# Kernel optimization log

Hardware: AMD Instinct MI355X
Metric: run time of the kernel (lower is better)

The kernel has to match this reference:

```python
import jax, jax.numpy as jnp
import numpy as np

HEADS = 16
DIM_HEAD = 64
EPS = 1e-8
MASK_VALUE = -np.finfo(np.float32).max


def rotate_half(x):
    # x: [..., rot_dim]; split into two halves (j=2 grouping) and rotate
    x1, x2 = jnp.split(x.reshape(*x.shape[:-1], 2, x.shape[-1] // 2), 2, axis=-2)
    x1 = x1.squeeze(-2)
    x2 = x2.squeeze(-2)
    return jnp.concatenate((-x2, x1), axis=-1)


def apply_rotary_pos_emb(t, freqs):
    # t: [b, h, n, d], freqs: [n, rot_dim]
    rot_dim = freqs.shape[-1]
    t_rot, t_pass = t[..., :rot_dim], t[..., rot_dim:]
    t_rot = t_rot * jnp.cos(freqs) + rotate_half(t_rot) * jnp.sin(freqs)
    return jnp.concatenate((t_rot, t_pass), axis=-1)


def setup_inputs() -> dict:
    key = jax.random.key(0)
    ks = jax.random.split(key, 6)
    b, n, dim = 2, 2048, 1024
    inner = HEADS * DIM_HEAD
    rot_dim = 32
    return {
        "x": jax.random.normal(ks[0], (b, n, dim), jnp.float32),
        "freqs": jax.random.normal(ks[1], (n, rot_dim), jnp.float32),
        "gamma": jnp.ones((dim,), jnp.float32),
        "Wq": jax.random.normal(ks[2], (dim, inner), jnp.float32) * (dim ** -0.5),
        "Wkv": jax.random.normal(ks[3], (dim, 2 * inner), jnp.float32) * (dim ** -0.5),
        "Wo": jax.random.normal(ks[4], (inner, dim), jnp.float32) * (inner ** -0.5),
        "bo": jnp.zeros((dim,), jnp.float32),
    }


def reference(x, freqs, gamma, Wq, Wkv, Wo, bo):
    b, n, dim = x.shape
    scale = DIM_HEAD ** -0.5

    # RMSNorm (norm-based formulation, matching the torch code)
    norm = jnp.linalg.norm(x, axis=-1, keepdims=True) * (dim ** -0.5)
    xn = x / jnp.maximum(norm, EPS) * gamma

    q = xn @ Wq                      # [b, n, h*d]
    kv = xn @ Wkv                    # [b, n, 2*h*d]
    k, v = jnp.split(kv, 2, axis=-1)

    def to_heads(t):
        return t.reshape(b, n, HEADS, DIM_HEAD).transpose(0, 2, 1, 3)  # [b,h,n,d]

    q, k, v = map(to_heads, (q, k, v))
    q = q * scale

    q = apply_rotary_pos_emb(q, freqs)
    k = apply_rotary_pos_emb(k, freqs)

    sim = jnp.einsum('bhid,bhjd->bhij', q, k)
    causal_mask = jnp.triu(jnp.ones((n, n), bool), k=1)
    sim = jnp.where(causal_mask, MASK_VALUE, sim)

    attn = jax.nn.softmax(sim, axis=-1)
    out = jnp.einsum('bhij,bhjd->bhid', attn, v)
    out = out.transpose(0, 2, 1, 3).reshape(b, n, HEADS * DIM_HEAD)
    return out @ Wo + bo
```

## Files before the change

### kernel.cpp

```cpp
#include <hip/hip_runtime.h>
#include <hip/hip_bf16.h>
#include <math.h>

typedef short s8 __attribute__((ext_vector_type(8)));
typedef float f4 __attribute__((ext_vector_type(4)));

#define HEADS 16
#define DHEAD 64
#define NSEQ 2048
#define BATCH 2
#define DIM 1024
#define ROT 32
#define QSCALE 0.18033688011112042f

static __device__ __forceinline__ unsigned short f2bf(float f) {
    union { float f; unsigned int u; } v; v.f = f;
    unsigned int u = v.u;
    unsigned int r = (u + 0x7FFFu + ((u >> 16) & 1u)) >> 16;
    return (unsigned short)r;
}

static __device__ __forceinline__ unsigned int cvt_pk_bf16(float lo, float hi) {
    unsigned int r;
    asm volatile("v_cvt_pk_bf16_f32 %0, %1, %2" : "=v"(r) : "v"(lo), "v"(hi));
    return r;
}

static __device__ __forceinline__ void gload_lds16(
        const unsigned short* g, unsigned short* l) {
    __builtin_amdgcn_global_load_lds(
        (const __attribute__((address_space(1))) void*)g,
        (__attribute__((address_space(3))) void*)l,
        16, 0, 0);
}

static __device__ __forceinline__ void tr_tile(
        const float* __restrict__ in, unsigned short* __restrict__ out,
        int K, int N, int n0, int k0, int tid, float* tile ) {
    int tx = tid & 31, ty = tid >> 5;
    #pragma unroll
    for (int j = 0; j < 32; j += 8)
        tile[(ty + j) * 33 + tx] = in[(size_t)(k0 + ty + j) * N + n0 + tx];
    __syncthreads();
    #pragma unroll
    for (int j = 0; j < 32; j += 8)
        out[(size_t)(n0 + ty + j) * K + k0 + tx] = f2bf(tile[tx * 33 + ty + j]);
}

__global__ __launch_bounds__(256) void prep_rms_kernel(
        const float* __restrict__ x, const float* __restrict__ gamma,
        const float* __restrict__ Wq, const float* __restrict__ Wkv,
        const float* __restrict__ Wo, const float* __restrict__ freqs,
        unsigned short* __restrict__ xn, unsigned short* __restrict__ WqT,
        unsigned short* __restrict__ WkvT, unsigned short* __restrict__ WoT,
        float* __restrict__ cs) {
    __shared__ float smem[32 * 33];
    int bid = blockIdx.x, tid = threadIdx.x;
    if (bid < 4096) {
        int row = bid;
        float4 v = ((const float4*)(x + (size_t)row * DIM))[tid];
        float ss = v.x * v.x + v.y * v.y + v.z * v.z + v.w * v.w;
        #pragma unroll
        for (int m = 1; m < 64; m <<= 1) ss += __shfl_xor(ss, m, 64);
        int wave = tid >> 6;
        if ((tid & 63) == 0) smem[wave] = ss;
        __syncthreads();
        float total = smem[0] + smem[1] + smem[2] + smem[3];
        float norm = sqrtf(total * (1.0f / DIM));
        float inv = 1.0f / fmaxf(norm, 1e-8f);
        float4 g = ((const float4*)gamma)[tid];
        ushort4 o;
        o.x = f2bf(v.x * inv * g.x);
        o.y = f2bf(v.y * inv * g.y);
        o.z = f2bf(v.z * inv * g.z);
        o.w = f2bf(v.w * inv * g.w);
        ((ushort4*)(xn + (size_t)row * DIM))[tid] = o;
    } else if (bid < 5120) {
        int idx = bid - 4096;
        tr_tile(Wq, WqT, 1024, 1024, (idx & 31) * 32, (idx >> 5) * 32, tid, smem);
    } else if (bid < 7168) {
        int idx = bid - 5120;
        tr_tile(Wkv, WkvT, 1024, 2048, (idx & 63) * 32, (idx >> 6) * 32, tid, smem);
    } else if (bid < 8192) {
        int idx = bid - 7168;
        tr_tile(Wo, WoT, 1024, 1024, (idx & 31) * 32, (idx >> 5) * 32, tid, smem);
    } else {
        int i = (bid - 8192) * 256 + tid;
        int npos = i >> 6, j = i & 63;
        int q = j >> 4;
        int fi = (q >> 1) * 16 + (j & 15);
        float f = freqs[npos * ROT + fi];
        cs[i] = (q & 1) ? sinf(f) : cosf(f);
    }
}

#define GEMM_COMPUTE(AOFF, BOFF)                                                        \
    {                                                                                   \
        s8 a0 = *(const s8*)(ar + (AOFF));                                              \
        s8 a1 = *(const s8*)(ar + (AOFF) + 512);                                        \
        s8 b0 = *(const s8*)(br + (BOFF));                                              \
        s8 b1 = *(const s8*)(br + (BOFF) + 512);                                        \
        s8 b2 = *(const s8*)(br + (BOFF) + 1024);                                       \
        s8 b3 = *(const s8*)(br + (BOFF) + 1536);                                       \
        acc[0][0] = __builtin_amdgcn_mfma_f32_16x16x32_bf16(a0, b0, acc[0][0], 0, 0, 0);\
        acc[0][1] = __builtin_amdgcn_mfma_f32_16x16x32_bf16(a0, b1, acc[0][1], 0, 0, 0);\
        acc[0][2] = __builtin_amdgcn_mfma_f32_16x16x32_bf16(a0, b2, acc[0][2], 0, 0, 0);\
        acc[0][3] = __builtin_amdgcn_mfma_f32_16x16x32_bf16(a0, b3, acc[0][3], 0, 0, 0);\
        acc[1][0] = __builtin_amdgcn_mfma_f32_16x16x32_bf16(a1, b0, acc[1][0], 0, 0, 0);\
        acc[1][1] = __builtin_amdgcn_mfma_f32_16x16x32_bf16(a1, b1, acc[1][1], 0, 0, 0);\
        acc[1][2] = __builtin_amdgcn_mfma_f32_16x16x32_bf16(a1, b2, acc[1][2], 0, 0, 0);\
        acc[1][3] = __builtin_amdgcn_mfma_f32_16x16x32_bf16(a1, b3, acc[1][3], 0, 0, 0);\
    }

#define GEMM_FENCE()                                             \
    asm volatile("s_waitcnt vmcnt(0)" ::: "memory");             \
    __builtin_amdgcn_s_barrier();                                \
    __builtin_amdgcn_sched_barrier(0);

static __device__ __forceinline__ void gemm_core64_db(
        const unsigned short* __restrict__ A, const unsigned short* __restrict__ BT,
        int bm0, int bn0, unsigned short* As, unsigned short* Bs, f4 acc[2][4]) {
    const int Kd = DIM;
    int tid = threadIdx.x, lane = tid & 63, w = tid >> 6;
    int wr = w >> 1, wc = w & 1;
    int r16 = lane & 15, g8 = 8 * (lane >> 4);
    int srow = lane >> 2, scol = (lane & 3) * 8;
    const unsigned short* Ag0 = A  + (size_t)(bm0 + w * 16 + srow) * Kd + scol;
    const unsigned short* Bg0 = BT + (size_t)(bn0 + (w * 2 + 0) * 16 + srow) * Kd + scol;
    const unsigned short* Bg1 = BT + (size_t)(bn0 + (w * 2 + 1) * 16 + srow) * Kd + scol;
    unsigned short* Al  = As + w * 512;
    unsigned short* Bl0 = Bs + (w * 2 + 0) * 512;
    unsigned short* Bl1 = Bs + (w * 2 + 1) * 512;
    const unsigned short* ar = As + (wr * 32 + r16) * 32 + g8;
    const unsigned short* br = Bs + (wc * 64 + r16) * 32 + g8;
    gload_lds16(Ag0, Al);
    gload_lds16(Bg0, Bl0);
    gload_lds16(Bg1, Bl1);
    GEMM_FENCE();
    for (int t = 0; t < 32; t += 2) {
        {
            int k1 = (t + 1) * 32;
            gload_lds16(Ag0 + k1, Al + 2048);
            gload_lds16(Bg0 + k1, Bl0 + 4096);
            gload_lds16(Bg1 + k1, Bl1 + 4096);
        }
        GEMM_COMPUTE(0, 0);
        GEMM_FENCE();
        if (t + 2 < 32) {
            int k2 = (t + 2) * 32;
            gload_lds16(Ag0 + k2, Al);
            gload_lds16(Bg0 + k2, Bl0);
            gload_lds16(Bg1 + k2, Bl1);
        }
        GEMM_COMPUTE(2048, 4096);
        GEMM_FENCE();
    }
}

__global__ __launch_bounds__(256) void gemm_qkv(
        const unsigned short* __restrict__ xn, const unsigned short* __restrict__ WqT,
        const unsigned short* __restrict__ WkvT, const float* __restrict__ cs,
        unsigned short* __restrict__ q_h, unsigned short* __restrict__ k_h,
        unsigned short* __restrict__ v_t) {
    __shared__ unsigned short As[2 * 64 * 32];
    __shared__ unsigned short Bs[2 * 128 * 32];
    f4 acc[2][4];
    #pragma unroll
    for (int m = 0; m < 2; ++m)
        #pragma unroll
        for (int n = 0; n < 4; ++n) acc[m][n] = 0.f;
    int bx = blockIdx.x;
    bool isq = (bx < 8);
    int bm0 = blockIdx.y * 64;
    int bn0 = (isq ? bx : (bx - 8)) * 128;
    gemm_core64_db(xn, isq ? WqT : WkvT, bm0, bn0, As, Bs, acc);
    int lane = threadIdx.x & 63, w = threadIdx.x >> 6;
    int wr = w >> 1, wc = w & 1, g = lane >> 4, c0 = lane & 15;
    if (isq) {
        int h = 2 * bx + wc;
        #pragma unroll
        for (int m = 0; m < 2; ++m)
            #pragma unroll
            for (int r = 0; r < 4; ++r) {
                int row = bm0 + wr * 32 + m * 16 + 4 * g + r;
                int b = row >> 11, npos = row & 2047;
                const float* csr = cs + npos * 64;
                float a0 = acc[m][0][r] * QSCALE;
                float a1 = acc[m][1][r] * QSCALE;
                float q0 = a0 * csr[c0] - a1 * csr[16 + c0];
                float q1 = a1 * csr[32 + c0] + a0 * csr[48 + c0];
                unsigned short* dst = q_h + ((size_t)(b * HEADS + h) * NSEQ + npos) * DHEAD;
                dst[c0]      = f2bf(q0);
                dst[16 + c0] = f2bf(q1);
                dst[32 + c0] = f2bf(acc[m][2][r] * QSCALE);
                dst[48 + c0] = f2bf(acc[m][3][r] * QSCALE);
            }
    } else if (bx < 16) {
        int h = 2 * (bx - 8) + wc;
        #pragma unroll
        for (int m = 0; m < 2; ++m)
            #pragma unroll
            for (int r = 0; r < 4; ++r) {
                int row = bm0 + wr * 32 + m * 16 + 4 * g + r;
                int b = row >> 11, npos = row & 2047;
                const float* csr = cs + npos * 64;
                float a0 = acc[m][0][r], a1 = acc[m][1][r];
                float k0v = a0 * csr[c0] - a1 * csr[16 + c0];
                float k1v = a1 * csr[32 + c0] + a0 * csr[48 + c0];
                unsigned short* dst = k_h + ((size_t)(b * HEADS + h) * NSEQ + npos) * DHEAD;
                dst[c0]      = f2bf(k0v);
                dst[16 + c0] = f2bf(k1v);
                dst[32 + c0] = f2bf(acc[m][2][r]);
                dst[48 + c0] = f2bf(acc[m][3][r]);
            }
    } else {
        int h = 2 * (bx - 16) + wc;
        #pragma unroll
        for (int m = 0; m < 2; ++m) {
            int row0 = bm0 + wr * 32 + m * 16 + 4 * g;
            int b = row0 >> 11, npos0 = row0 & 2047;
            unsigned short* vb = v_t + (size_t)(b * HEADS + h) * DHEAD * NSEQ;
            #pragma unroll
            for (int n = 0; n < 4; ++n) {
                uint2 pk;
                pk.x = cvt_pk_bf16(acc[m][n][0], acc[m][n][1]);
                pk.y = cvt_pk_bf16(acc[m][n][2], acc[m][n][3]);
                *(uint2*)(vb + (size_t)(n * 16 + c0) * NSEQ + npos0) = pk;
            }
        }
    }
}

#define PSTRIDE 72

static __device__ __forceinline__ void stage_kv64(
        const unsigned short* __restrict__ kb, const unsigned short* __restrict__ vb,
        int j0, unsigned short* Kd, unsigned short* Vd, int w, int lane) {
    int r8 = lane >> 3, c = lane & 7;
    int sc = c ^ r8;
    #pragma unroll
    for (int i = 0; i < 2; ++i) {
        int rb = (w * 2 + i) * 8;
        int r = rb + r8;
        gload_lds16(kb + (size_t)(j0 + r) * DHEAD + sc * 8, Kd + rb * DHEAD);
        gload_lds16(vb + (size_t)r * NSEQ + j0 + sc * 8,    Vd + rb * DHEAD);
    }
}

template<bool MASKT>
static __device__ __forceinline__ void attn_tile_lds(
        int j0, int q0, int g, int c0, int njt,
        const unsigned short* Kc, const unsigned short* Vc,
        s8 qf0, s8 qf1, unsigned short* plw,
        f4 o[4], float& m, float& l) {
    int sw = c0 & 7;
    int off0 = ((g ^ sw) << 3);
    int off1 = (((g + 4) ^ sw) << 3);
    f4 s[4];
    #pragma unroll
    for (int jt = 0; jt < 4; ++jt) {
        f4 acc; acc = 0.f;
        if (!MASKT || jt < njt) {
            const unsigned short* kp = Kc + (jt * 16 + c0) * DHEAD;
            s8 kf0 = *(const s8*)(kp + off0);
            s8 kf1 = *(const s8*)(kp + off1);
            acc = __builtin_amdgcn_mfma_f32_16x16x32_bf16(kf0, qf0, acc, 0, 0, 0);
            acc = __builtin_amdgcn_mfma_f32_16x16x32_bf16(kf1, qf1, acc, 0, 0, 0);
        }
        s[jt] = acc;
    }
    if (MASKT) {
        #pragma unroll
        for (int jt = 0; jt < 4; ++jt)
            #pragma unroll
            for (int r = 0; r < 4; ++r) {
                int j = j0 + jt * 16 + 4 * g + r;
                if (j > q0 + c0) s[jt][r] = -1e30f;
            }
    }
    f4 mv = s[0];
    #pragma unroll
    for (int jt = 1; jt < 4; ++jt)
        #pragma unroll
        for (int r = 0; r < 4; ++r) mv[r] = fmaxf(mv[r], s[jt][r]);
    float mx = fmaxf(fmaxf(mv[0], mv[1]), fmaxf(mv[2], mv[3]));
    mx = fmaxf(mx, __shfl_xor(mx, 16));
    mx = fmaxf(mx, __shfl_xor(mx, 32));
    if (__any(mx > m + 11.5f)) {
        float mnew = fmaxf(m, mx);
        float alpha = exp2f(m - mnew);
        l *= alpha;
        #pragma unroll
        for (int dc = 0; dc < 4; ++dc)
            #pragma unroll
            for (int r = 0; r < 4; ++r) o[dc][r] *= alpha;
        m = mnew;
    }
    float rs = 0.f;
    unsigned int* prow = (unsigned int*)(plw + c0 * PSTRIDE);
    #pragma unroll
    for (int jt = 0; jt < 4; ++jt) {
        f4 p;
        #pragma unroll
        for (int r = 0; r < 4; ++r) { p[r] = exp2f(s[jt][r] - m); rs += p[r]; }
        uint2 pk;
        pk.x = cvt_pk_bf16(p[0], p[1]);
        pk.y = cvt_pk_bf16(p[2], p[3]);
        ((uint2*)prow)[jt * 4 + g] = pk;
    }
    rs += __shfl_xor(rs, 16);
    rs += __shfl_xor(rs, 32);
    l += rs;
    __builtin_amdgcn_sched_barrier(0);
    asm volatile("s_waitcnt lgkmcnt(0)" ::: "memory");
    __builtin_amdgcn_sched_barrier(0);
    const unsigned short* prd = plw + c0 * PSTRIDE + 8 * g;
    s8 pf0 = *(const s8*)(prd);
    s8 pf1 = *(const s8*)(prd + 32);
    bool hi_half = (!MASKT) || (njt > 2);
    #pragma unroll
    for (int dc = 0; dc < 4; ++dc) {
        const unsigned short* vp = Vc + (dc * 16 + c0) * DHEAD;
        s8 vf0 = *(const s8*)(vp + off0);
        o[dc] = __builtin_amdgcn_mfma_f32_16x16x32_bf16(vf0, pf0, o[dc], 0, 0, 0);
        if (hi_half) {
            s8 vf1 = *(const s8*)(vp + off1);
            o[dc] = __builtin_amdgcn_mfma_f32_16x16x32_bf16(vf1, pf1, o[dc], 0, 0, 0);
        }
    }
}

__global__ __launch_bounds__(256) void attn_kernel(
        const unsigned short* __restrict__ q_h, const unsigned short* __restrict__ k_h,
        const unsigned short* __restrict__ v_t, unsigned short* __restrict__ attn_out) {
    __shared__ unsigned short Ks[2][64 * DHEAD];
    __shared__ unsigned short Vs[2][64 * DHEAD];
    __shared__ unsigned short p_lds[4][16][PSTRIDE];
    int tid = threadIdx.x, lane = tid & 63, w = tid >> 6;
    int g = lane >> 4, c0 = lane & 15;
    int bid = blockIdx.x;
    int k = bid >> 3;
    int qt = 31 - (k >> 2);
    int bh = (bid & 7) + ((k & 3) << 3);
    const unsigned short* qb = q_h + (size_t)bh * NSEQ * DHEAD;
    const unsigned short* kb = k_h + (size_t)bh * NSEQ * DHEAD;
    const unsigned short* vb = v_t + (size_t)bh * DHEAD * NSEQ;
    unsigned short* plw = &p_lds[w][0][0];
    int b = bh >> 4, h = bh & 15;
    int q0 = qt * 64 + w * 16;
    s8 qf0 = *(const s8*)(qb + (size_t)(q0 + c0) * DHEAD + 8 * g);
    s8 qf1 = *(const s8*)(qb + (size_t)(q0 + c0) * DHEAD + 32 + 8 * g);
    f4 o[4]; o[0] = 0.f; o[1] = 0.f; o[2] = 0.f; o[3] = 0.f;
    float m = -1e30f, l = 0.f;
    int nt = qt + 1;
    stage_kv64(kb, vb, 0, Ks[0], Vs[0], w, lane);
    __syncthreads();
    for (int t = 0; t < nt; ++t) {
        const unsigned short* Kc = Ks[t & 1];
        const unsigned short* Vc = Vs[t & 1];
        if (t + 1 < nt)
            stage_kv64(kb, vb, (t + 1) * 64, Ks[(t + 1) & 1], Vs[(t + 1) & 1], w, lane);
        if (t == nt - 1)
            attn_tile_lds<true>(t * 64, q0, g, c0, w + 1, Kc, Vc, qf0, qf1, plw, o, m, l);
        else
            attn_tile_lds<false>(t * 64, q0, g, c0, 4, Kc, Vc, qf0, qf1, plw, o, m, l);
        __syncthreads();
    }
    float invl = 1.0f / l;
    unsigned short* dst = attn_out + ((size_t)(b * NSEQ) + q0 + c0) * (HEADS * DHEAD) + h * DHEAD;
    #pragma unroll
    for (int dc = 0; dc < 4; ++dc) {
        uint2 pk;
        pk.x = cvt_pk_bf16(o[dc][0] * invl, o[dc][1] * invl);
        pk.y = cvt_pk_bf16(o[dc][2] * invl, o[dc][3] * invl);
        *(uint2*)(dst + dc * 16 + 4 * g) = pk;
    }
}

__global__ __launch_bounds__(256) void gemm_o(
        const unsigned short* __restrict__ attn, const unsigned short* __restrict__ WoT,
        const float* __restrict__ bo, float* __restrict__ out) {
    __shared__ unsigned short As[2 * 64 * 32];
    __shared__ unsigned short Bs[2 * 128 * 32];
    f4 acc[2][4];
    #pragma unroll
    for (int m = 0; m < 2; ++m)
        #pragma unroll
        for (int n = 0; n < 4; ++n) acc[m][n] = 0.f;
    int bm0 = blockIdx.y * 64, bn0 = blockIdx.x * 128;
    gemm_core64_db(attn, WoT, bm0, bn0, As, Bs, acc);
    int lane = threadIdx.x & 63, w = threadIdx.x >> 6;
    int wr = w >> 1, wc = w & 1, g = lane >> 4, c0 = lane & 15;
    #pragma unroll
    for (int m = 0; m < 2; ++m)
        #pragma unroll
        for (int r = 0; r < 4; ++r) {
            int row = bm0 + wr * 32 + m * 16 + 4 * g + r;
            #pragma unroll
            for (int n = 0; n < 4; ++n) {
                int col = bn0 + wc * 64 + n * 16 + c0;
                out[(size_t)row * DIM + col] = acc[m][n][r] + bo[col];
            }
        }
}

extern "C" void kernel_launch(void* const* d_in, const int* in_sizes, int n_in,
                              void* d_out, int out_size, void* d_ws, size_t ws_size,
                              hipStream_t stream) {
    const float* x     = (const float*)d_in[0];
    const float* freqs = (const float*)d_in[1];
    const float* gamma = (const float*)d_in[2];
    const float* Wq    = (const float*)d_in[3];
    const float* Wkv   = (const float*)d_in[4];
    const float* Wo    = (const float*)d_in[5];
    const float* bo    = (const float*)d_in[6];
    float* out = (float*)d_out;

    char* ws = (char*)d_ws;
    unsigned short* xn   = (unsigned short*)(ws + 0);
    unsigned short* WqT  = (unsigned short*)(ws + 8388608);
    unsigned short* WkvT = (unsigned short*)(ws + 10485760);
    unsigned short* WoT  = (unsigned short*)(ws + 14680064);
    unsigned short* q_h  = (unsigned short*)(ws + 16777216);
    unsigned short* k_h  = (unsigned short*)(ws + 25165824);
    unsigned short* v_t  = (unsigned short*)(ws + 33554432);
    float*          cs   = (float*)(ws + 41943040);
    unsigned short* attn = xn;

    prep_rms_kernel<<<8704, 256, 0, stream>>>(x, gamma, Wq, Wkv, Wo, freqs,
                                              xn, WqT, WkvT, WoT, cs);
    gemm_qkv<<<dim3(24, 64), 256, 0, stream>>>(xn, WqT, WkvT, cs, q_h, k_h, v_t);
    attn_kernel<<<1024, 256, 0, stream>>>(q_h, k_h, v_t, attn);
    gemm_o  <<<dim3(8, 64), 256, 0, stream>>>(attn, WoT, bo, out);
}
```

Baseline: 133.6 us.

## Triple-buffer GEMM K-loop and compute softmax row sums with MFMA

The shared GEMM core moves from a double-buffered LDS pipeline to a three-stage one. It keeps two K-tiles in flight, uses partial vmcnt waits, and fully unrolls the 32-step loop, so global-load latency is hidden better than with the per-step vmcnt(0) fence. In attention, the per-row softmax denominator is now accumulated by an MFMA of a ones vector against the P fragments, replacing the scalar adds and cross-lane shuffles. The costs are 50% more LDS per GEMM block, which may reduce occupancy, larger unrolled code, and one or two extra MFMAs per attention tile.

```diff
diff --git a/kernel.cpp b/kernel.cpp
--- a/kernel.cpp
+++ b/kernel.cpp
@@ -94,30 +94,7 @@
     }
 }
 
-#define GEMM_COMPUTE(AOFF, BOFF)                                                        \
-    {                                                                                   \
-        s8 a0 = *(const s8*)(ar + (AOFF));                                              \
-        s8 a1 = *(const s8*)(ar + (AOFF) + 512);                                        \
-        s8 b0 = *(const s8*)(br + (BOFF));                                              \
-        s8 b1 = *(const s8*)(br + (BOFF) + 512);                                        \
-        s8 b2 = *(const s8*)(br + (BOFF) + 1024);                                       \
-        s8 b3 = *(const s8*)(br + (BOFF) + 1536);                                       \
-        acc[0][0] = __builtin_amdgcn_mfma_f32_16x16x32_bf16(a0, b0, acc[0][0], 0, 0, 0);\
-        acc[0][1] = __builtin_amdgcn_mfma_f32_16x16x32_bf16(a0, b1, acc[0][1], 0, 0, 0);\
-        acc[0][2] = __builtin_amdgcn_mfma_f32_16x16x32_bf16(a0, b2, acc[0][2], 0, 0, 0);\
-        acc[0][3] = __builtin_amdgcn_mfma_f32_16x16x32_bf16(a0, b3, acc[0][3], 0, 0, 0);\
-        acc[1][0] = __builtin_amdgcn_mfma_f32_16x16x32_bf16(a1, b0, acc[1][0], 0, 0, 0);\
-        acc[1][1] = __builtin_amdgcn_mfma_f32_16x16x32_bf16(a1, b1, acc[1][1], 0, 0, 0);\
-        acc[1][2] = __builtin_amdgcn_mfma_f32_16x16x32_bf16(a1, b2, acc[1][2], 0, 0, 0);\
-        acc[1][3] = __builtin_amdgcn_mfma_f32_16x16x32_bf16(a1, b3, acc[1][3], 0, 0, 0);\
-    }
-
-#define GEMM_FENCE()                                             \
-    asm volatile("s_waitcnt vmcnt(0)" ::: "memory");             \
-    __builtin_amdgcn_s_barrier();                                \
-    __builtin_amdgcn_sched_barrier(0);
-
-static __device__ __forceinline__ void gemm_core64_db(
+static __device__ __forceinline__ void gemm_core64_p3(
         const unsigned short* __restrict__ A, const unsigned short* __restrict__ BT,
         int bm0, int bn0, unsigned short* As, unsigned short* Bs, f4 acc[2][4]) {
     const int Kd = DIM;
@@ -133,27 +110,52 @@
     unsigned short* Bl1 = Bs + (w * 2 + 1) * 512;
     const unsigned short* ar = As + (wr * 32 + r16) * 32 + g8;
     const unsigned short* br = Bs + (wc * 64 + r16) * 32 + g8;
-    gload_lds16(Ag0, Al);
-    gload_lds16(Bg0, Bl0);
-    gload_lds16(Bg1, Bl1);
-    GEMM_FENCE();
-    for (int t = 0; t < 32; t += 2) {
+    #pragma unroll
+    for (int p = 0; p < 3; ++p) {
+        int k0 = p * 32;
+        gload_lds16(Ag0 + k0, Al + p * 2048);
+        gload_lds16(Bg0 + k0, Bl0 + p * 4096);
+        gload_lds16(Bg1 + k0, Bl1 + p * 4096);
+    }
+    asm volatile("s_waitcnt vmcnt(6)" ::: "memory");
+    __builtin_amdgcn_s_barrier();
+    __builtin_amdgcn_sched_barrier(0);
+    #pragma unroll
+    for (int t = 0; t < 32; ++t) {
+        const int cb = t % 3;
+        const int aoff = cb * 2048;
+        const int boff = cb * 4096;
         {
-            int k1 = (t + 1) * 32;
-            gload_lds16(Ag0 + k1, Al + 2048);
-            gload_lds16(Bg0 + k1, Bl0 + 4096);
-            gload_lds16(Bg1 + k1, Bl1 + 4096);
-        }
-        GEMM_COMPUTE(0, 0);
-        GEMM_FENCE();
-        if (t + 2 < 32) {
-            int k2 = (t + 2) * 32;
-            gload_lds16(Ag0 + k2, Al);
-            gload_lds16(Bg0 + k2, Bl0);
-            gload_lds16(Bg1 + k2, Bl1);
-        }
-        GEMM_COMPUTE(2048, 4096);
-        GEMM_FENCE();
+            s8 a0 = *(const s8*)(ar + aoff);
+            s8 a1 = *(const s8*)(ar + aoff + 512);
+            s8 b0 = *(const s8*)(br + boff);
+            s8 b1 = *(const s8*)(br + boff + 512);
+            s8 b2 = *(const s8*)(br + boff + 1024);
+            s8 b3 = *(const s8*)(br + boff + 1536);
+            acc[0][0] = __builtin_amdgcn_mfma_f32_16x16x32_bf16(a0, b0, acc[0][0], 0, 0, 0);
+            acc[0][1] = __builtin_amdgcn_mfma_f32_16x16x32_bf16(a0, b1, acc[0][1], 0, 0, 0);
+            acc[0][2] = __builtin_amdgcn_mfma_f32_16x16x32_bf16(a0, b2, acc[0][2], 0, 0, 0);
+            acc[0][3] = __builtin_amdgcn_mfma_f32_16x16x32_bf16(a0, b3, acc[0][3], 0, 0, 0);
+            acc[1][0] = __builtin_amdgcn_mfma_f32_16x16x32_bf16(a1, b0, acc[1][0], 0, 0, 0);
+            acc[1][1] = __builtin_amdgcn_mfma_f32_16x16x32_bf16(a1, b1, acc[1][1], 0, 0, 0);
+            acc[1][2] = __builtin_amdgcn_mfma_f32_16x16x32_bf16(a1, b2, acc[1][2], 0, 0, 0);
+            acc[1][3] = __builtin_amdgcn_mfma_f32_16x16x32_bf16(a1, b3, acc[1][3], 0, 0, 0);
+        }
+        __builtin_amdgcn_sched_barrier(0);
+        __builtin_amdgcn_s_barrier();
+        if (t + 3 < 32) {
+            int k3 = (t + 3) * 32;
+            gload_lds16(Ag0 + k3, Al + aoff);
+            gload_lds16(Bg0 + k3, Bl0 + boff);
+            gload_lds16(Bg1 + k3, Bl1 + boff);
+        }
+        if (t + 1 < 32) {
+            if (t + 3 < 32)      { asm volatile("s_waitcnt vmcnt(6)" ::: "memory"); }
+            else if (t + 2 < 32) { asm volatile("s_waitcnt vmcnt(3)" ::: "memory"); }
+            else                 { asm volatile("s_waitcnt vmcnt(0)" ::: "memory"); }
+            __builtin_amdgcn_s_barrier();
+            __builtin_amdgcn_sched_barrier(0);
+        }
     }
 }
 
@@ -162,8 +164,8 @@
         const unsigned short* __restrict__ WkvT, const float* __restrict__ cs,
         unsigned short* __restrict__ q_h, unsigned short* __restrict__ k_h,
         unsigned short* __restrict__ v_t) {
-    __shared__ unsigned short As[2 * 64 * 32];
-    __shared__ unsigned short Bs[2 * 128 * 32];
+    __shared__ unsigned short As[3 * 64 * 32];
+    __shared__ unsigned short Bs[3 * 128 * 32];
     f4 acc[2][4];
     #pragma unroll
     for (int m = 0; m < 2; ++m)
@@ -173,7 +175,7 @@
     bool isq = (bx < 8);
     int bm0 = blockIdx.y * 64;
     int bn0 = (isq ? bx : (bx - 8)) * 128;
-    gemm_core64_db(xn, isq ? WqT : WkvT, bm0, bn0, As, Bs, acc);
+    gemm_core64_p3(xn, isq ? WqT : WkvT, bm0, bn0, As, Bs, acc);
     int lane = threadIdx.x & 63, w = threadIdx.x >> 6;
     int wr = w >> 1, wc = w & 1, g = lane >> 4, c0 = lane & 15;
     if (isq) {
@@ -252,7 +254,7 @@
         int j0, int q0, int g, int c0, int njt,
         const unsigned short* Kc, const unsigned short* Vc,
         s8 qf0, s8 qf1, unsigned short* plw,
-        f4 o[4], float& m, float& l) {
+        f4 o[4], float& m, f4& ol) {
     int sw = c0 & 7;
     int off0 = ((g ^ sw) << 3);
     int off1 = (((g + 4) ^ sw) << 3);
@@ -278,39 +280,35 @@
                 if (j > q0 + c0) s[jt][r] = -1e30f;
             }
     }
-    f4 mv = s[0];
-    #pragma unroll
-    for (int jt = 1; jt < 4; ++jt)
-        #pragma unroll
-        for (int r = 0; r < 4; ++r) mv[r] = fmaxf(mv[r], s[jt][r]);
+    f4 mv;
+    #pragma unroll
+    for (int r = 0; r < 4; ++r)
+        mv[r] = fmaxf(fmaxf(s[0][r], s[1][r]), fmaxf(s[2][r], s[3][r]));
     float mx = fmaxf(fmaxf(mv[0], mv[1]), fmaxf(mv[2], mv[3]));
     mx = fmaxf(mx, __shfl_xor(mx, 16));
     mx = fmaxf(mx, __shfl_xor(mx, 32));
     if (__any(mx > m + 11.5f)) {
         float mnew = fmaxf(m, mx);
         float alpha = exp2f(m - mnew);
-        l *= alpha;
         #pragma unroll
         for (int dc = 0; dc < 4; ++dc)
             #pragma unroll
             for (int r = 0; r < 4; ++r) o[dc][r] *= alpha;
+        #pragma unroll
+        for (int r = 0; r < 4; ++r) ol[r] *= alpha;
         m = mnew;
     }
-    float rs = 0.f;
     unsigned int* prow = (unsigned int*)(plw + c0 * PSTRIDE);
     #pragma unroll
     for (int jt = 0; jt < 4; ++jt) {
         f4 p;
         #pragma unroll
-        for (int r = 0; r < 4; ++r) { p[r] = exp2f(s[jt][r] - m); rs += p[r]; }
+        for (int r = 0; r < 4; ++r) p[r] = exp2f(s[jt][r] - m);
         uint2 pk;
         pk.x = cvt_pk_bf16(p[0], p[1]);
         pk.y = cvt_pk_bf16(p[2], p[3]);
         ((uint2*)prow)[jt * 4 + g] = pk;
     }
-    rs += __shfl_xor(rs, 16);
-    rs += __shfl_xor(rs, 32);
-    l += rs;
     __builtin_amdgcn_sched_barrier(0);
     asm volatile("s_waitcnt lgkmcnt(0)" ::: "memory");
     __builtin_amdgcn_sched_barrier(0);
@@ -318,6 +316,11 @@
     s8 pf0 = *(const s8*)(prd);
     s8 pf1 = *(const s8*)(prd + 32);
     bool hi_half = (!MASKT) || (njt > 2);
+    const s8 onesf = {(short)0x3F80, (short)0x3F80, (short)0x3F80, (short)0x3F80,
+                      (short)0x3F80, (short)0x3F80, (short)0x3F80, (short)0x3F80};
+    ol = __builtin_amdgcn_mfma_f32_16x16x32_bf16(onesf, pf0, ol, 0, 0, 0);
+    if (hi_half)
+        ol = __builtin_amdgcn_mfma_f32_16x16x32_bf16(onesf, pf1, ol, 0, 0, 0);
     #pragma unroll
     for (int dc = 0; dc < 4; ++dc) {
         const unsigned short* vp = Vc + (dc * 16 + c0) * DHEAD;
@@ -351,7 +354,8 @@
     s8 qf0 = *(const s8*)(qb + (size_t)(q0 + c0) * DHEAD + 8 * g);
     s8 qf1 = *(const s8*)(qb + (size_t)(q0 + c0) * DHEAD + 32 + 8 * g);
     f4 o[4]; o[0] = 0.f; o[1] = 0.f; o[2] = 0.f; o[3] = 0.f;
-    float m = -1e30f, l = 0.f;
+    f4 ol; ol = 0.f;
+    float m = -1e30f;
     int nt = qt + 1;
     stage_kv64(kb, vb, 0, Ks[0], Vs[0], w, lane);
     __syncthreads();
@@ -361,12 +365,12 @@
         if (t + 1 < nt)
             stage_kv64(kb, vb, (t + 1) * 64, Ks[(t + 1) & 1], Vs[(t + 1) & 1], w, lane);
         if (t == nt - 1)
-            attn_tile_lds<true>(t * 64, q0, g, c0, w + 1, Kc, Vc, qf0, qf1, plw, o, m, l);
+            attn_tile_lds<true>(t * 64, q0, g, c0, w + 1, Kc, Vc, qf0, qf1, plw, o, m, ol);
         else
-            attn_tile_lds<false>(t * 64, q0, g, c0, 4, Kc, Vc, qf0, qf1, plw, o, m, l);
+            attn_tile_lds<false>(t * 64, q0, g, c0, 4, Kc, Vc, qf0, qf1, plw, o, m, ol);
         __syncthreads();
     }
-    float invl = 1.0f / l;
+    float invl = 1.0f / ol[0];
     unsigned short* dst = attn_out + ((size_t)(b * NSEQ) + q0 + c0) * (HEADS * DHEAD) + h * DHEAD;
     #pragma unroll
     for (int dc = 0; dc < 4; ++dc) {
@@ -380,15 +384,15 @@
 __global__ __launch_bounds__(256) void gemm_o(
         const unsigned short* __restrict__ attn, const unsigned short* __restrict__ WoT,
         const float* __restrict__ bo, float* __restrict__ out) {
-    __shared__ unsigned short As[2 * 64 * 32];
-    __shared__ unsigned short Bs[2 * 128 * 32];
+    __shared__ unsigned short As[3 * 64 * 32];
+    __shared__ unsigned short Bs[3 * 128 * 32];
     f4 acc[2][4];
     #pragma unroll
     for (int m = 0; m < 2; ++m)
         #pragma unroll
         for (int n = 0; n < 4; ++n) acc[m][n] = 0.f;
     int bm0 = blockIdx.y * 64, bn0 = blockIdx.x * 128;
-    gemm_core64_db(attn, WoT, bm0, bn0, As, Bs, acc);
+    gemm_core64_p3(attn, WoT, bm0, bn0, As, Bs, acc);
     int lane = threadIdx.x & 63, w = threadIdx.x >> 6;
     int wr = w >> 1, wc = w & 1, g = lane >> 4, c0 = lane & 15;
     #pragma unroll
```

New measurement: 127.6 us. -4.5%, faster.
